# Optimization experiments

Measured on AMD Instinct MI355X. Metric: run time of the kernel, lower is better.

## Reference

```python
import jax, jax.numpy as jnp
import numpy as np

D, NH, NL, NP, NLAYERS, DFF = 256, 8, 4, 4, 6, 1024
HD = D // NH
SHAPES = [(100, 100), (50, 50), (25, 25), (13, 13)]  # (H, W) per level
B = 4


def layernorm(x, w, b):
    m = x.mean(-1, keepdims=True)
    v = ((x - m) ** 2).mean(-1, keepdims=True)
    return (x - m) / jnp.sqrt(v + 1e-5) * w + b


def bilinear_sample(vl, loc, H, W):
    # vl: [B, H*W, NH, HD] level values; loc: [B, Lq, NH, NP, 2] normalized in [0,1]
    # matches F.grid_sample(bilinear, zeros padding, align_corners=False)
    bsz, Lq = loc.shape[0], loc.shape[1]
    px = loc[..., 0] * W - 0.5
    py = loc[..., 1] * H - 0.5
    x0 = jnp.floor(px); y0 = jnp.floor(py)
    wx1 = px - x0; wy1 = py - y0
    out = jnp.zeros((bsz, Lq, NH, NP, HD), vl.dtype)
    for xi, wx in ((x0, 1.0 - wx1), (x0 + 1.0, wx1)):
        for yi, wy in ((y0, 1.0 - wy1), (y0 + 1.0, wy1)):
            valid = (xi >= 0) & (xi < W) & (yi >= 0) & (yi < H)
            xc = jnp.clip(xi, 0, W - 1).astype(jnp.int32)
            yc = jnp.clip(yi, 0, H - 1).astype(jnp.int32)
            idx = yc * W + xc                                   # [B,Lq,NH,NP]
            idx2 = idx.transpose(0, 1, 3, 2).reshape(bsz, Lq * NP, NH, 1)
            g = jnp.take_along_axis(vl, idx2, axis=1)           # [B,Lq*NP,NH,HD]
            g = g.reshape(bsz, Lq, NP, NH, HD).transpose(0, 1, 3, 2, 4)
            w = (wx * wy * valid.astype(vl.dtype))[..., None]
            out = out + g * w
    return out


def get_reference_points(bsz):
    refs = []
    for (H, W) in SHAPES:
        ry = (jnp.arange(H, dtype=jnp.float32) + 0.5) / H
        rx = (jnp.arange(W, dtype=jnp.float32) + 0.5) / W
        gy, gx = jnp.meshgrid(ry, rx, indexing='ij')
        refs.append(jnp.stack([gx.reshape(-1), gy.reshape(-1)], -1))
    ref = jnp.concatenate(refs, 0)                              # [Len, 2]
    return jnp.broadcast_to(ref[None, :, None, :], (bsz, ref.shape[0], NL, 2))


def ms_deform_attn(query, src, ref, starts, so_w, so_b, aw_w, aw_b, vp_w, vp_b, op_w, op_b):
    bsz, Lq, _ = query.shape
    value = (src @ vp_w + vp_b).reshape(bsz, -1, NH, HD)
    offsets = (query @ so_w + so_b).reshape(bsz, Lq, NH, NL, NP, 2)
    aw = (query @ aw_w + aw_b).reshape(bsz, Lq, NH, NL * NP)
    aw = jax.nn.softmax(aw, -1).reshape(bsz, Lq, NH, NL, NP)
    normalizer = jnp.array([[W, H] for (H, W) in SHAPES], jnp.float32)  # x by W, y by H
    loc = ref[:, :, None, :, None, :] + offsets / normalizer[None, None, None, :, None, :]
    out = jnp.zeros((bsz, Lq, NH, HD), query.dtype)
    for l, (H, W) in enumerate(SHAPES):
        vl = value[:, starts[l]:starts[l] + H * W]
        sampled = bilinear_sample(vl, loc[:, :, :, l], H, W)    # [B,Lq,NH,NP,HD]
        out = out + jnp.einsum('blhp,blhpd->blhd', aw[:, :, :, l], sampled)
    return out.reshape(bsz, Lq, D) @ op_w + op_b


def setup_inputs():
    key = jax.random.key(0)
    ks = iter(jax.random.split(key, 64))
    d = {}
    for i, (H, W) in enumerate(SHAPES):
        d[f'src{i}'] = jax.random.normal(next(ks), (B, D, H, W), jnp.float32)
        d[f'pos{i}'] = jax.random.normal(next(ks), (B, D, H, W), jnp.float32)
    d['level_embed'] = jax.random.normal(next(ks), (NL, D), jnp.float32)
    d['so_w'] = jax.random.normal(next(ks), (NLAYERS, D, NH * NL * NP * 2), jnp.float32) * 0.005
    d['so_b'] = jax.random.normal(next(ks), (NLAYERS, NH * NL * NP * 2), jnp.float32) * 0.1
    d['aw_w'] = jax.random.normal(next(ks), (NLAYERS, D, NH * NL * NP), jnp.float32) * 0.02
    d['aw_b'] = jnp.zeros((NLAYERS, NH * NL * NP), jnp.float32)
    d['vp_w'] = jax.random.normal(next(ks), (NLAYERS, D, D), jnp.float32) * 0.02
    d['vp_b'] = jnp.zeros((NLAYERS, D), jnp.float32)
    d['op_w'] = jax.random.normal(next(ks), (NLAYERS, D, D), jnp.float32) * 0.02
    d['op_b'] = jnp.zeros((NLAYERS, D), jnp.float32)
    d['n1_w'] = jnp.ones((NLAYERS, D), jnp.float32)
    d['n1_b'] = jnp.zeros((NLAYERS, D), jnp.float32)
    d['f1_w'] = jax.random.normal(next(ks), (NLAYERS, D, DFF), jnp.float32) * 0.02
    d['f1_b'] = jnp.zeros((NLAYERS, DFF), jnp.float32)
    d['f2_w'] = jax.random.normal(next(ks), (NLAYERS, DFF, D), jnp.float32) * 0.02
    d['f2_b'] = jnp.zeros((NLAYERS, D), jnp.float32)
    d['n2_w'] = jnp.ones((NLAYERS, D), jnp.float32)
    d['n2_b'] = jnp.zeros((NLAYERS, D), jnp.float32)
    return d


def reference(src0, src1, src2, src3, pos0, pos1, pos2, pos3, level_embed,
              so_w, so_b, aw_w, aw_b, vp_w, vp_b, op_w, op_b,
              n1_w, n1_b, f1_w, f1_b, f2_w, f2_b, n2_w, n2_b):
    srcs = [src0, src1, src2, src3]
    poss = [pos0, pos1, pos2, pos3]
    bsz = src0.shape[0]
    src_flat, pos_flat, starts, off = [], [], [], 0
    for l, ((H, W), s, p) in enumerate(zip(SHAPES, srcs, poss)):
        starts.append(off); off += H * W
        src_flat.append(s.reshape(bsz, D, H * W).transpose(0, 2, 1))
        pos_flat.append(p.reshape(bsz, D, H * W).transpose(0, 2, 1) + level_embed[l][None, None, :])
    src = jnp.concatenate(src_flat, 1)                          # [B, Len, D]
    pos = jnp.concatenate(pos_flat, 1)
    ref = get_reference_points(bsz)
    for i in range(NLAYERS):
        q = src + pos
        attn = ms_deform_attn(q, src, ref, starts,
                              so_w[i], so_b[i], aw_w[i], aw_b[i],
                              vp_w[i], vp_b[i], op_w[i], op_b[i])
        src = layernorm(src + attn, n1_w[i], n1_b[i])
        h = jax.nn.relu(src @ f1_w[i] + f1_b[i]) @ f2_w[i] + f2_b[i]
        src = layernorm(src + h, n2_w[i], n2_b[i])
    level_start_index = jnp.array(starts, jnp.int64 if jax.config.jax_enable_x64 else jnp.int32)
    return src, level_start_index
```

## Files before the change

### kernel.cpp

```cpp
#include <hip/hip_runtime.h>

#define D 256
#define L_TOT 13294

typedef __attribute__((ext_vector_type(8))) __bf16 bf16x8;
typedef __attribute__((ext_vector_type(4))) float f32x4;
typedef __attribute__((ext_vector_type(2))) float f32x2;

__device__ __forceinline__ float bf2f(unsigned short u) {
    return __uint_as_float(((unsigned int)u) << 16);
}
__device__ __forceinline__ unsigned short f2bf(float f) {
    unsigned int u = __float_as_uint(f);
    u += 0x7FFFu + ((u >> 16) & 1u);
    return (unsigned short)(u >> 16);
}
__device__ __forceinline__ f32x2 bfpair(unsigned int d) {
    f32x2 r;
    r.x = __uint_as_float(d << 16);
    r.y = __uint_as_float(d & 0xFFFF0000u);
    return r;
}
__device__ __forceinline__ f32x2 fma2(f32x2 a, float w, f32x2 c) {
    return __builtin_elementwise_fma(a, (f32x2){w, w}, c);
}

__global__ void probe_k(const unsigned short* __restrict__ u, int n, int* __restrict__ flag)
{
    __shared__ int cnt;
    if (threadIdx.x == 0) cnt = 0;
    __syncthreads();
    int c = 0;
    for (int i = threadIdx.x; i < n; i += 256) {
        const int e = (u[i] >> 7) & 0xFF;
        if (e == 0 || (e >= 96 && e <= 150)) ++c;
    }
    atomicAdd(&cnt, c);
    __syncthreads();
    if (threadIdx.x == 0) *flag = (cnt * 10 > n * 9) ? 1 : 0;
}

__global__ __launch_bounds__(256) void convert_k(
    const void* __restrict__ src, unsigned short* __restrict__ dst, int n,
    const int* __restrict__ flag)
{
    const int i = blockIdx.x * 256 + threadIdx.x;
    if (i >= n) return;
    if (*flag) dst[i] = ((const unsigned short*)src)[i];
    else       dst[i] = f2bf(((const float*)src)[i]);
}

__global__ __launch_bounds__(256) void convt_k(
    const void* __restrict__ src, unsigned short* __restrict__ dst,
    int K, int N, int L, const int* __restrict__ flag)
{
    const long e = (long)blockIdx.x * 256 + threadIdx.x;
    const long tot = (long)L * K * N;
    if (e >= tot) return;
    const int per = K * N;
    const int li = (int)(e / per);
    const int r  = (int)(e - (long)li * per);
    const int n  = r / K;
    const int k  = r - n * K;
    const long s = (long)li * per + (long)k * N + n;
    dst[e] = (*flag) ? ((const unsigned short*)src)[s]
                     : f2bf(((const float*)src)[s]);
}

__global__ __launch_bounds__(256) void flatten_k(
    const void* __restrict__ s0, const void* __restrict__ s1,
    const void* __restrict__ s2, const void* __restrict__ s3,
    const int* __restrict__ flag, unsigned short* __restrict__ state)
{
    const long e = (long)blockIdx.x * 256 + threadIdx.x;
    const int d = (int)(e & 255);
    const long tok = e >> 8;
    const int b = (int)(tok / L_TOT);
    const int t = (int)(tok - (long)b * L_TOT);
    const void *sp;
    int hw, idx;
    if (t < 10000)      { sp = s0; hw = 10000; idx = t;          }
    else if (t < 12500) { sp = s1; hw = 2500;  idx = t - 10000;  }
    else if (t < 13125) { sp = s2; hw = 625;   idx = t - 12500;  }
    else                { sp = s3; hw = 169;   idx = t - 13125;  }
    const long a = ((long)b * D + d) * hw + idx;
    state[e] = (*flag) ? ((const unsigned short*)sp)[a]
                       : f2bf(((const float*)sp)[a]);
}

__global__ __launch_bounds__(256) void posconst_k(
    const void* __restrict__ p0, const void* __restrict__ p1,
    const void* __restrict__ p2, const void* __restrict__ p3,
    const unsigned short* __restrict__ lev, const int* __restrict__ flag,
    unsigned short* __restrict__ posc)
{
    const long e = (long)blockIdx.x * 256 + threadIdx.x;
    const int d = (int)(e & 255);
    const long tok = e >> 8;
    const int b = (int)(tok / L_TOT);
    const int t = (int)(tok - (long)b * L_TOT);
    const void *pp;
    int hw, idx, l;
    if (t < 10000)      { pp = p0; hw = 10000; idx = t;          l = 0; }
    else if (t < 12500) { pp = p1; hw = 2500;  idx = t - 10000;  l = 1; }
    else if (t < 13125) { pp = p2; hw = 625;   idx = t - 12500;  l = 2; }
    else                { pp = p3; hw = 169;   idx = t - 13125;  l = 3; }
    const long a = ((long)b * D + d) * hw + idx;
    const float pv = (*flag) ? bf2f(((const unsigned short*)pp)[a])
                             : ((const float*)pp)[a];
    posc[e] = f2bf(pv + bf2f(lev[l * D + d]));
}

__global__ __launch_bounds__(256) void addq_k(
    const unsigned short* __restrict__ x, const unsigned short* __restrict__ p,
    unsigned short* __restrict__ q, long n8)
{
    const long e = (long)blockIdx.x * 256 + threadIdx.x;
    if (e >= n8) return;
    const uint4 xv = ((const uint4*)x)[e];
    const uint4 pv = ((const uint4*)p)[e];
    uint4 o;
#define ADDPK(a, b) ({ const f32x2 fa = bfpair(a), fb = bfpair(b); \
        (unsigned int)f2bf(fb.x + fa.x) | ((unsigned int)f2bf(fb.y + fa.y) << 16); })
    o.x = ADDPK(xv.x, pv.x); o.y = ADDPK(xv.y, pv.y);
    o.z = ADDPK(xv.z, pv.z); o.w = ADDPK(xv.w, pv.w);
#undef ADDPK
    ((uint4*)q)[e] = o;
}

__global__ __launch_bounds__(256) void posflat_k(
    const void* __restrict__ p0, const void* __restrict__ p1,
    const void* __restrict__ p2, const void* __restrict__ p3,
    const unsigned short* __restrict__ lev, const int* __restrict__ flag,
    const unsigned short* __restrict__ x, unsigned short* __restrict__ q)
{
    const long e = (long)blockIdx.x * 256 + threadIdx.x;
    const int d = (int)(e & 255);
    const long tok = e >> 8;
    const int b = (int)(tok / L_TOT);
    const int t = (int)(tok - (long)b * L_TOT);
    const void *pp;
    int hw, idx, l;
    if (t < 10000)      { pp = p0; hw = 10000; idx = t;          l = 0; }
    else if (t < 12500) { pp = p1; hw = 2500;  idx = t - 10000;  l = 1; }
    else if (t < 13125) { pp = p2; hw = 625;   idx = t - 12500;  l = 2; }
    else                { pp = p3; hw = 169;   idx = t - 13125;  l = 3; }
    const long a = ((long)b * D + d) * hw + idx;
    const float pv = (*flag) ? bf2f(((const unsigned short*)pp)[a])
                             : ((const float*)pp)[a];
    q[e] = f2bf(pv + bf2f(lev[l * D + d]) + bf2f(x[e]));
}

template<bool RELU, bool RESID>
__device__ __forceinline__ void gemm_core(
    const unsigned short* __restrict__ A, int ldA,
    const unsigned short* __restrict__ Bt, int ldB,
    const unsigned short* __restrict__ bias,
    const unsigned short* resid,
    unsigned short* out, int ldO,
    long M, int K, int col0, long row0,
    unsigned short* As, unsigned short* Bs)
{
    const int tid = threadIdx.x;
    const int l  = tid & 63;
    const int w  = tid >> 6;
    const int wm = w >> 1, wn = w & 1;

    f32x4 acc[4][4];
#pragma unroll
    for (int i = 0; i < 4; ++i)
#pragma unroll
        for (int j = 0; j < 4; ++j) acc[i][j] = (f32x4){0.f, 0.f, 0.f, 0.f};

    const int sr = tid >> 3;
    const int sg = tid & 7;

    for (int k0 = 0; k0 < K; k0 += 64) {
#pragma unroll
        for (int i = 0; i < 4; ++i) {
            const int r = i * 32 + sr;
            long arow = row0 + r; if (arow >= M) arow = M - 1;
            const int ke = k0 + ((sg ^ (r & 7)) << 3);
            const unsigned short* ga = A  + arow * (long)ldA + ke;
            const unsigned short* gb = Bt + (long)(col0 + r) * ldB + ke;
            __builtin_amdgcn_global_load_lds(
                (const __attribute__((address_space(1))) void*)ga,
                (__attribute__((address_space(3))) void*)(As + i * 2048 + w * 512),
                16, 0, 0);
            __builtin_amdgcn_global_load_lds(
                (const __attribute__((address_space(1))) void*)gb,
                (__attribute__((address_space(3))) void*)(Bs + i * 2048 + w * 512),
                16, 0, 0);
        }
        __syncthreads();
#pragma unroll
        for (int ks = 0; ks < 2; ++ks) {
            const int cc  = ks * 4 + (l >> 4);
            const int swz = ((cc ^ (l & 7)) << 4);
            bf16x8 af[4], bfr[4];
#pragma unroll
            for (int mi = 0; mi < 4; ++mi) {
                const int ar = wm * 64 + mi * 16 + (l & 15);
                af[mi] = *(const bf16x8*)((const char*)As + ar * 128 + swz);
            }
#pragma unroll
            for (int ni = 0; ni < 4; ++ni) {
                const int br = wn * 64 + ni * 16 + (l & 15);
                bfr[ni] = *(const bf16x8*)((const char*)Bs + br * 128 + swz);
            }
#pragma unroll
            for (int mi = 0; mi < 4; ++mi)
#pragma unroll
                for (int ni = 0; ni < 4; ++ni)
                    acc[mi][ni] = __builtin_amdgcn_mfma_f32_16x16x32_bf16(
                        bfr[ni], af[mi], acc[mi][ni], 0, 0, 0);
        }
        __syncthreads();
    }

#pragma unroll
    for (int mi = 0; mi < 4; ++mi) {
        const long rr = row0 + wm * 64 + mi * 16 + (l & 15);
        if (rr >= M) continue;
#pragma unroll
        for (int ni = 0; ni < 4; ++ni) {
            const int col = col0 + wn * 64 + ni * 16 + (l >> 4) * 4;
            f32x4 v = acc[mi][ni];
            if (bias) {
                const ushort4 b4 = *(const ushort4*)(bias + col);
                v[0] += bf2f(b4.x); v[1] += bf2f(b4.y);
                v[2] += bf2f(b4.z); v[3] += bf2f(b4.w);
            }
            if (RELU) {
                v[0] = fmaxf(v[0], 0.f); v[1] = fmaxf(v[1], 0.f);
                v[2] = fmaxf(v[2], 0.f); v[3] = fmaxf(v[3], 0.f);
            }
            if (RESID) {
                const ushort4 r4 = *(const ushort4*)(resid + rr * (long)ldO + col);
                v[0] += bf2f(r4.x); v[1] += bf2f(r4.y);
                v[2] += bf2f(r4.z); v[3] += bf2f(r4.w);
            }
            ushort4 o;
            o.x = f2bf(v[0]); o.y = f2bf(v[1]); o.z = f2bf(v[2]); o.w = f2bf(v[3]);
            *(ushort4*)(out + rr * (long)ldO + col) = o;
        }
    }
}

template<bool RELU, bool RESID>
__global__ __launch_bounds__(256, 3) void mgemm_k(
    const unsigned short* __restrict__ A, int ldA,
    const unsigned short* __restrict__ Bt, int ldB,
    const unsigned short* __restrict__ bias,
    const unsigned short* resid,
    unsigned short* out, int ldOut,
    long M, int K)
{
    __shared__ unsigned short As[8192];
    __shared__ unsigned short Bs[8192];
    gemm_core<RELU, RESID>(A, ldA, Bt, ldB, bias, resid, out, ldOut,
                           M, K, blockIdx.x * 128, (long)blockIdx.y * 128, As, Bs);
}

__global__ __launch_bounds__(256, 3) void mgemm3_k(
    const unsigned short* __restrict__ state, const unsigned short* __restrict__ q,
    const unsigned short* __restrict__ Wv,  const unsigned short* __restrict__ bv,
    const unsigned short* __restrict__ Wso, const unsigned short* __restrict__ bso,
    const unsigned short* __restrict__ Waw, const unsigned short* __restrict__ baw,
    unsigned short* valo, unsigned short* offo, unsigned short* awo, long M)
{
    __shared__ unsigned short As[8192];
    __shared__ unsigned short Bs[8192];
    const int cx = blockIdx.x * 128;
    const long row0 = (long)blockIdx.y * 128;
    if (cx < 256)
        gemm_core<false, false>(state, D, Wv, D, bv, nullptr, valo, D,
                                M, D, cx, row0, As, Bs);
    else if (cx < 512)
        gemm_core<false, false>(q, D, Wso, D, bso, nullptr, offo, D,
                                M, D, cx - 256, row0, As, Bs);
    else
        gemm_core<false, false>(q, D, Waw, D, baw, nullptr, awo, 128,
                                M, D, 0, row0, As, Bs);
}

__global__ __launch_bounds__(256) void sample_k(
    const unsigned short* __restrict__ off, const unsigned short* __restrict__ aw,
    const unsigned short* __restrict__ val, unsigned short* __restrict__ attn)
{
    __shared__ __align__(16) int   cidx[128][4];
    __shared__ __align__(16) float cw[128][4];
    __shared__ float red[3][4][64];
    const long tok = blockIdx.x;
    const int tid = threadIdx.x;
    const int b = (int)(tok / L_TOT);
    const int t = (int)(tok - (long)b * L_TOT);

    if (tid < 128) {
        const int u = tid;
        const int lp = u & 15;
        const int mu = lp * 8 + (u >> 4);
        const int cswz = lp & 3;
        const float logit = bf2f(aw[tok * 128 + u]);
        float m = logit;
#pragma unroll
        for (int mk = 1; mk < 16; mk <<= 1) m = fmaxf(m, __shfl_xor(m, mk));
        const float e = expf(logit - m);
        float s = e;
#pragma unroll
        for (int mk = 1; mk < 16; mk <<= 1) s += __shfl_xor(s, mk);
        const float a = e / s;
        int st0, W0;
        if (t < 10000)      { st0 = 0;     W0 = 100; }
        else if (t < 12500) { st0 = 10000; W0 = 50;  }
        else if (t < 13125) { st0 = 12500; W0 = 25;  }
        else                { st0 = 13125; W0 = 13;  }
        const int i0 = t - st0;
        const int yy = i0 / W0;
        const int xx = i0 - yy * W0;
        const float gx = (xx + 0.5f) / (float)W0;
        const float gy = (yy + 0.5f) / (float)W0;
        const int lv = (u >> 2) & 3;
        const int Wv  = (lv == 0) ? 100 : (lv == 1) ? 50 : (lv == 2) ? 25 : 13;
        const int stl = (lv == 0) ? 0 : (lv == 1) ? 10000 : (lv == 2) ? 12500 : 13125;
        const unsigned int op = *(const unsigned int*)(off + tok * 256 + 2 * u);
        const float ox = bf2f((unsigned short)op);
        const float oy = bf2f((unsigned short)(op >> 16));
        const float px = (gx + ox / (float)Wv) * Wv - 0.5f;
        const float py = (gy + oy / (float)Wv) * Wv - 0.5f;
        const float fx = floorf(px), fy = floorf(py);
        const float wx1 = px - fx, wy1 = py - fy;
        const int x0 = (int)fx, y0 = (int)fy;
#pragma unroll
        for (int c = 0; c < 4; ++c) {
            const int xi = x0 + (c & 1);
            const int yi = y0 + (c >> 1);
            const float wgt = ((c & 1) ? wx1 : 1.f - wx1) * ((c >> 1) ? wy1 : 1.f - wy1);
            const bool ok = (xi >= 0) && (xi < Wv) && (yi >= 0) && (yi < Wv);
            cidx[mu][c ^ cswz] = ok ? ((stl + yi * Wv + xi) << 9) : 0;
            cw[mu][c ^ cswz]   = ok ? wgt * a : 0.f;
        }
    }
    __syncthreads();
    const int g = tid >> 6;
    const int l = tid & 63;
    const int h = l >> 3;
    const int q = l & 7;
    const char* vb = (const char*)val + ((long)b * L_TOT) * 512 + h * 64 + q * 8;
    f32x2 A01 = {0.f, 0.f}, A23 = {0.f, 0.f};
#pragma unroll
    for (int j = 0; j < 4; ++j) {
        const int mu = (j * 4 + g) * 8 + h;
        const int4   ci = *(const int4*)(&cidx[mu][0]);
        const float4 wv = *(const float4*)(&cw[mu][0]);
        const uint2 d0 = *(const uint2*)(vb + ci.x);
        const uint2 d1 = *(const uint2*)(vb + ci.y);
        const uint2 d2 = *(const uint2*)(vb + ci.z);
        const uint2 d3 = *(const uint2*)(vb + ci.w);
        A01 = fma2(bfpair(d0.x), wv.x, A01);  A23 = fma2(bfpair(d0.y), wv.x, A23);
        A01 = fma2(bfpair(d1.x), wv.y, A01);  A23 = fma2(bfpair(d1.y), wv.y, A23);
        A01 = fma2(bfpair(d2.x), wv.z, A01);  A23 = fma2(bfpair(d2.y), wv.z, A23);
        A01 = fma2(bfpair(d3.x), wv.w, A01);  A23 = fma2(bfpair(d3.y), wv.w, A23);
    }
    if (g) {
        red[g - 1][0][l] = A01.x; red[g - 1][1][l] = A01.y;
        red[g - 1][2][l] = A23.x; red[g - 1][3][l] = A23.y;
    }
    __syncthreads();
    if (g == 0) {
        float a0 = A01.x, a1 = A01.y, a2 = A23.x, a3 = A23.y;
#pragma unroll
        for (int p = 0; p < 3; ++p) {
            a0 += red[p][0][l]; a1 += red[p][1][l];
            a2 += red[p][2][l]; a3 += red[p][3][l];
        }
        ushort4 o;
        o.x = f2bf(a0); o.y = f2bf(a1); o.z = f2bf(a2); o.w = f2bf(a3);
        *(ushort4*)(attn + tok * 256 + h * 32 + q * 4) = o;
    }
}

template<bool QOUT>
__global__ __launch_bounds__(256) void ln_k(
    const unsigned short* __restrict__ y,
    const unsigned short* __restrict__ g, const unsigned short* __restrict__ bb,
    unsigned short* __restrict__ out,
    const unsigned short* __restrict__ posc, unsigned short* __restrict__ qout,
    long nt)
{
    const int wv = threadIdx.x >> 6;
    const int lane = threadIdx.x & 63;
    const long tok = (long)blockIdx.x * 4 + wv;
    if (tok >= nt) return;
    const ushort4 v4 = *(const ushort4*)(y + tok * D + lane * 4);
    const float v0 = bf2f(v4.x), v1 = bf2f(v4.y), v2 = bf2f(v4.z), v3 = bf2f(v4.w);
    float s = v0 + v1 + v2 + v3;
#pragma unroll
    for (int m = 1; m < 64; m <<= 1) s += __shfl_xor(s, m);
    const float mean = s * (1.f / D);
    const float d0 = v0 - mean, d1 = v1 - mean, d2 = v2 - mean, d3 = v3 - mean;
    float q = d0 * d0 + d1 * d1 + d2 * d2 + d3 * d3;
#pragma unroll
    for (int m = 1; m < 64; m <<= 1) q += __shfl_xor(q, m);
    const float rstd = rsqrtf(q * (1.f / D) + 1e-5f);
    const int c0 = lane * 4;
    ushort4 o;
    o.x = f2bf(d0 * rstd * bf2f(g[c0 + 0]) + bf2f(bb[c0 + 0]));
    o.y = f2bf(d1 * rstd * bf2f(g[c0 + 1]) + bf2f(bb[c0 + 1]));
    o.z = f2bf(d2 * rstd * bf2f(g[c0 + 2]) + bf2f(bb[c0 + 2]));
    o.w = f2bf(d3 * rstd * bf2f(g[c0 + 3]) + bf2f(bb[c0 + 3]));
    *(ushort4*)(out + tok * D + c0) = o;
    if (QOUT) {
        const ushort4 p4 = *(const ushort4*)(posc + tok * D + c0);
        ushort4 qo;
        qo.x = f2bf(bf2f(o.x) + bf2f(p4.x));
        qo.y = f2bf(bf2f(o.y) + bf2f(p4.y));
        qo.z = f2bf(bf2f(o.z) + bf2f(p4.z));
        qo.w = f2bf(bf2f(o.w) + bf2f(p4.w));
        *(ushort4*)(qout + tok * D + c0) = qo;
    }
}

__global__ __launch_bounds__(256) void finalize_k(
    const unsigned short* __restrict__ state, float* __restrict__ out, long osz)
{
    const long e = (long)blockIdx.x * 256 + threadIdx.x;
    const long n0 = osz - 4;
    if (e < n0) out[e] = bf2f(state[e]);
    if (e < 4) {
        const float st[4] = {0.f, 10000.f, 12500.f, 13125.f};
        out[n0 + e] = st[e];
    }
}

extern "C" void kernel_launch(void* const* d_in, const int* in_sizes, int n_in,
                              void* d_out, int out_size, void* d_ws, size_t ws_size,
                              hipStream_t stream)
{
    (void)n_in;
    const long osz = (long)out_size;
    const long nt = (osz - 4) / D;
    const int nlayers = in_sizes[9] / (D * D);
    const int dff = in_sizes[19] / (nlayers * D);

    char* ws = (char*)d_ws;
    int* flag = (int*)ws;  ws += 256;
    unsigned short* wc = (unsigned short*)ws;
    long off[25]; long acc_off = 0;
    for (int i = 8; i <= 24; ++i) { off[i] = acc_off; acc_off += in_sizes[i]; }
    ws += ((acc_off * 2 + 255) / 256) * 256;
    const size_t SZ_BF = (size_t)nt * D * 2;
    unsigned short* state     = (unsigned short*)ws;  ws += SZ_BF;
    unsigned short* val_b     = (unsigned short*)ws;  ws += SZ_BF;
    unsigned short* offy_b    = (unsigned short*)ws;  ws += SZ_BF;
    unsigned short* posattn_b = (unsigned short*)ws;  ws += SZ_BF;
    unsigned short* aw_b      = (unsigned short*)ws;  ws += (size_t)nt * 128 * 2;
    unsigned short* hbuf = val_b;

    const size_t used_base = (size_t)((char*)aw_b - (char*)d_ws) + (size_t)nt * 128 * 2;
    const bool have_posc  = (ws_size >= used_base + SZ_BF);
    const bool have_hfull = (ws_size >= used_base + SZ_BF + 4 * SZ_BF);
    unsigned short* posc  = (unsigned short*)((char*)d_ws + used_base);
    unsigned short* hfull = (unsigned short*)((char*)d_ws + used_base + SZ_BF);

    probe_k<<<1, 256, 0, stream>>>((const unsigned short*)d_in[8], in_sizes[8], flag);

    const int vecIdx[11] = {8, 10, 12, 14, 16, 17, 18, 20, 22, 23, 24};
    for (int j = 0; j < 11; ++j) {
        const int i = vecIdx[j];
        convert_k<<<(in_sizes[i] + 255) / 256, 256, 0, stream>>>(
            d_in[i], wc + off[i], in_sizes[i], flag);
    }
    const int matIdx[6] = {9, 11, 13, 15, 19, 21};
    const int matK[6]   = {D, D, D, D, D, dff};
    const int matN[6]   = {D, 128, D, D, dff, D};
    for (int j = 0; j < 6; ++j) {
        const int i = matIdx[j];
        convt_k<<<(in_sizes[i] + 255) / 256, 256, 0, stream>>>(
            d_in[i], wc + off[i], matK[j], matN[j], nlayers, flag);
    }

    flatten_k<<<(int)nt, 256, 0, stream>>>(
        d_in[0], d_in[2], d_in[4], d_in[6], flag, state);
    if (have_posc)
        posconst_k<<<(int)nt, 256, 0, stream>>>(
            d_in[1], d_in[3], d_in[5], d_in[7], wc + off[8], flag, posc);

    const int MB = (int)((nt + 127) / 128);
    const int LB = (int)((nt + 3) / 4);
    const long n8 = (long)nt * D / 8;
    const int AB = (int)((n8 + 255) / 256);
    const int dh = dff / 2;

    if (have_posc)
        addq_k<<<AB, 256, 0, stream>>>(state, posc, posattn_b, n8);

    for (int i = 0; i < nlayers; ++i) {
        if (!have_posc)
            posflat_k<<<(int)nt, 256, 0, stream>>>(
                d_in[1], d_in[3], d_in[5], d_in[7], wc + off[8], flag, state, posattn_b);
        mgemm3_k<<<dim3(5, MB), 256, 0, stream>>>(
            state, posattn_b,
            wc + off[13] + (long)i * D * D,   wc + off[14] + i * D,
            wc + off[9]  + (long)i * D * 256, wc + off[10] + i * 256,
            wc + off[11] + (long)i * D * 128, wc + off[12] + i * 128,
            val_b, offy_b, aw_b, nt);
        sample_k<<<(int)nt, 256, 0, stream>>>(offy_b, aw_b, val_b, posattn_b);
        mgemm_k<false, true><<<dim3(2, MB), 256, 0, stream>>>(
            posattn_b, D, wc + off[15] + (long)i * D * D, D, wc + off[16] + i * D,
            state, offy_b, D, nt, D);
        ln_k<false><<<LB, 256, 0, stream>>>(offy_b, wc + off[17] + i * D,
            wc + off[18] + i * D, state, nullptr, nullptr, nt);
        if (have_hfull) {
            mgemm_k<true, false><<<dim3(dff / 128, MB), 256, 0, stream>>>(
                state, D, wc + off[19] + (long)i * D * dff, D, wc + off[20] + i * dff,
                nullptr, hfull, dff, nt, D);
            mgemm_k<false, true><<<dim3(2, MB), 256, 0, stream>>>(
                hfull, dff, wc + off[21] + (long)i * dff * D, dff, wc + off[22] + i * D,
                state, posattn_b, D, nt, dff);
        } else {
            mgemm_k<true, false><<<dim3(dh / 128, MB), 256, 0, stream>>>(
                state, D, wc + off[19] + (long)i * D * dff, D, wc + off[20] + i * dff,
                nullptr, hbuf, dh, nt, D);
            mgemm_k<false, true><<<dim3(2, MB), 256, 0, stream>>>(
                hbuf, dh, wc + off[21] + (long)i * dff * D, dff, wc + off[22] + i * D,
                state, posattn_b, D, nt, dh);
            mgemm_k<true, false><<<dim3(dh / 128, MB), 256, 0, stream>>>(
                state, D, wc + off[19] + (long)i * D * dff + (long)dh * D, D,
                wc + off[20] + i * dff + dh, nullptr, hbuf, dh, nt, D);
            mgemm_k<false, true><<<dim3(2, MB), 256, 0, stream>>>(
                hbuf, dh, wc + off[21] + (long)i * dff * D + dh, dff, nullptr,
                posattn_b, posattn_b, D, nt, dh);
        }
        if (have_posc && i + 1 < nlayers)
            ln_k<true><<<LB, 256, 0, stream>>>(posattn_b, wc + off[23] + i * D,
                wc + off[24] + i * D, state, posc, posattn_b, nt);
        else
            ln_k<false><<<LB, 256, 0, stream>>>(posattn_b, wc + off[23] + i * D,
                wc + off[24] + i * D, state, nullptr, nullptr, nt);
    }

    finalize_k<<<(int)((osz - 4 + 255) / 256), 256, 0, stream>>>(
        state, (float*)d_out, osz);
}
```

Baseline: 2.479 ms.

## Fuse output-projection and FFN2 GEMMs with residual add and LayerNorm

Adds a GEMM kernel whose 64-row tiles span the full 256-wide output, so the residual add and LayerNorm (plus the optional pos-add for the next layer's query) run in the epilogue. It replaces the separate GEMM and ln_k launches on the hfull path. This removes the round trip of the intermediate activation through global memory and two launches per layer. The cost is fewer blocks with a large B tile held in LDS. Reading resid and writing outp in place on the same state buffer relies on each block touching only its own rows.

Measured after the change: 2.406 ms. -2.9%, faster.

```diff
diff --git a/kernel.cpp b/kernel.cpp
--- a/kernel.cpp
+++ b/kernel.cpp
@@ -282,6 +282,149 @@
     else
         gemm_core<false, false>(q, D, Waw, D, baw, nullptr, awo, 128,
                                 M, D, 0, row0, As, Bs);
+}
+
+template<bool QOUT>
+__global__ __launch_bounds__(256, 3) void mgemmln_k(
+    const unsigned short* __restrict__ A, int ldA,
+    const unsigned short* __restrict__ Bt, int ldB,
+    const unsigned short* __restrict__ bias,
+    const unsigned short* resid,
+    const unsigned short* __restrict__ gamma,
+    const unsigned short* __restrict__ beta,
+    unsigned short* outp,
+    const unsigned short* __restrict__ posc,
+    unsigned short* __restrict__ qout,
+    long M, int K)
+{
+    __shared__ unsigned short As[64 * 64];
+    __shared__ unsigned short Bs[256 * 64];
+    __shared__ float red[2][4][4][16];
+    const int tid = threadIdx.x;
+    const int l = tid & 63;
+    const int w = tid >> 6;
+    const long row0 = (long)blockIdx.x * 64;
+
+    f32x4 acc[4][4];
+#pragma unroll
+    for (int i = 0; i < 4; ++i)
+#pragma unroll
+        for (int j = 0; j < 4; ++j) acc[i][j] = (f32x4){0.f, 0.f, 0.f, 0.f};
+
+    for (int k0 = 0; k0 < K; k0 += 64) {
+#pragma unroll
+        for (int i = 0; i < 10; ++i) {
+            const int c = i * 256 + tid;
+            const unsigned short* gsrc;
+            unsigned short* ldst;
+            if (i < 2) {
+                const int r = c >> 3, grp = c & 7;
+                long ar = row0 + r; if (ar >= M) ar = M - 1;
+                gsrc = A + ar * (long)ldA + (k0 + ((grp ^ (r & 7)) << 3));
+                ldst = As + (c << 3);
+            } else {
+                const int r = (c >> 3) - 64, grp = c & 7;
+                gsrc = Bt + (long)r * ldB + (k0 + ((grp ^ (r & 7)) << 3));
+                ldst = Bs + ((c - 512) << 3);
+            }
+            __builtin_amdgcn_global_load_lds(
+                (const __attribute__((address_space(1))) void*)gsrc,
+                (__attribute__((address_space(3))) void*)ldst, 16, 0, 0);
+        }
+        __syncthreads();
+#pragma unroll
+        for (int ks = 0; ks < 2; ++ks) {
+            const int cc = ks * 4 + (l >> 4);
+            bf16x8 af[4], bfr[4];
+#pragma unroll
+            for (int mi = 0; mi < 4; ++mi) {
+                const int ar = mi * 16 + (l & 15);
+                af[mi] = *(const bf16x8*)((const char*)As + ar * 128 + ((cc ^ (ar & 7)) << 4));
+            }
+#pragma unroll
+            for (int ni = 0; ni < 4; ++ni) {
+                const int br = w * 64 + ni * 16 + (l & 15);
+                bfr[ni] = *(const bf16x8*)((const char*)Bs + br * 128 + ((cc ^ (br & 7)) << 4));
+            }
+#pragma unroll
+            for (int mi = 0; mi < 4; ++mi)
+#pragma unroll
+                for (int ni = 0; ni < 4; ++ni)
+                    acc[mi][ni] = __builtin_amdgcn_mfma_f32_16x16x32_bf16(
+                        bfr[ni], af[mi], acc[mi][ni], 0, 0, 0);
+        }
+        __syncthreads();
+    }
+
+#pragma unroll
+    for (int mi = 0; mi < 4; ++mi) {
+        const long rr = row0 + mi * 16 + (l & 15);
+        const long rrc = (rr < M) ? rr : (M - 1);
+#pragma unroll
+        for (int ni = 0; ni < 4; ++ni) {
+            const int col = w * 64 + ni * 16 + (l >> 4) * 4;
+            const ushort4 b4 = *(const ushort4*)(bias + col);
+            const ushort4 r4 = *(const ushort4*)(resid + rrc * D + col);
+            acc[mi][ni][0] = bf2f(f2bf(acc[mi][ni][0] + bf2f(b4.x) + bf2f(r4.x)));
+            acc[mi][ni][1] = bf2f(f2bf(acc[mi][ni][1] + bf2f(b4.y) + bf2f(r4.y)));
+            acc[mi][ni][2] = bf2f(f2bf(acc[mi][ni][2] + bf2f(b4.z) + bf2f(r4.z)));
+            acc[mi][ni][3] = bf2f(f2bf(acc[mi][ni][3] + bf2f(b4.w) + bf2f(r4.w)));
+        }
+    }
+#pragma unroll
+    for (int mi = 0; mi < 4; ++mi) {
+        float s = 0.f, qq = 0.f;
+#pragma unroll
+        for (int ni = 0; ni < 4; ++ni)
+#pragma unroll
+            for (int r = 0; r < 4; ++r) {
+                const float v = acc[mi][ni][r];
+                s += v; qq += v * v;
+            }
+        s += __shfl_xor(s, 16);  s += __shfl_xor(s, 32);
+        qq += __shfl_xor(qq, 16); qq += __shfl_xor(qq, 32);
+        if (l < 16) { red[0][w][mi][l] = s; red[1][w][mi][l] = qq; }
+    }
+    __syncthreads();
+    float mean[4], rstd[4];
+#pragma unroll
+    for (int mi = 0; mi < 4; ++mi) {
+        const int r16 = l & 15;
+        const float s = red[0][0][mi][r16] + red[0][1][mi][r16]
+                      + red[0][2][mi][r16] + red[0][3][mi][r16];
+        const float qq = red[1][0][mi][r16] + red[1][1][mi][r16]
+                       + red[1][2][mi][r16] + red[1][3][mi][r16];
+        const float mn = s * (1.f / D);
+        const float var = qq * (1.f / D) - mn * mn;
+        mean[mi] = mn;
+        rstd[mi] = rsqrtf(var + 1e-5f);
+    }
+#pragma unroll
+    for (int mi = 0; mi < 4; ++mi) {
+        const long rr = row0 + mi * 16 + (l & 15);
+        if (rr >= M) continue;
+#pragma unroll
+        for (int ni = 0; ni < 4; ++ni) {
+            const int col = w * 64 + ni * 16 + (l >> 4) * 4;
+            const ushort4 g4 = *(const ushort4*)(gamma + col);
+            const ushort4 e4 = *(const ushort4*)(beta + col);
+            ushort4 o;
+            o.x = f2bf((acc[mi][ni][0] - mean[mi]) * rstd[mi] * bf2f(g4.x) + bf2f(e4.x));
+            o.y = f2bf((acc[mi][ni][1] - mean[mi]) * rstd[mi] * bf2f(g4.y) + bf2f(e4.y));
+            o.z = f2bf((acc[mi][ni][2] - mean[mi]) * rstd[mi] * bf2f(g4.z) + bf2f(e4.z));
+            o.w = f2bf((acc[mi][ni][3] - mean[mi]) * rstd[mi] * bf2f(g4.w) + bf2f(e4.w));
+            *(ushort4*)(outp + rr * D + col) = o;
+            if (QOUT) {
+                const ushort4 p4 = *(const ushort4*)(posc + rr * D + col);
+                ushort4 qo;
+                qo.x = f2bf(bf2f(o.x) + bf2f(p4.x));
+                qo.y = f2bf(bf2f(o.y) + bf2f(p4.y));
+                qo.z = f2bf(bf2f(o.z) + bf2f(p4.z));
+                qo.w = f2bf(bf2f(o.w) + bf2f(p4.w));
+                *(ushort4*)(qout + rr * D + col) = qo;
+            }
+        }
+    }
 }
 
 __global__ __launch_bounds__(256) void sample_k(
@@ -487,6 +630,7 @@
             d_in[1], d_in[3], d_in[5], d_in[7], wc + off[8], flag, posc);
 
     const int MB = (int)((nt + 127) / 128);
+    const int FB = (int)((nt + 63) / 64);
     const int LB = (int)((nt + 3) / 4);
     const long n8 = (long)nt * D / 8;
     const int AB = (int)((n8 + 255) / 256);
@@ -506,19 +650,32 @@
             wc + off[11] + (long)i * D * 128, wc + off[12] + i * 128,
             val_b, offy_b, aw_b, nt);
         sample_k<<<(int)nt, 256, 0, stream>>>(offy_b, aw_b, val_b, posattn_b);
-        mgemm_k<false, true><<<dim3(2, MB), 256, 0, stream>>>(
-            posattn_b, D, wc + off[15] + (long)i * D * D, D, wc + off[16] + i * D,
-            state, offy_b, D, nt, D);
-        ln_k<false><<<LB, 256, 0, stream>>>(offy_b, wc + off[17] + i * D,
-            wc + off[18] + i * D, state, nullptr, nullptr, nt);
         if (have_hfull) {
+            mgemmln_k<false><<<FB, 256, 0, stream>>>(
+                posattn_b, D, wc + off[15] + (long)i * D * D, D, wc + off[16] + i * D,
+                state, wc + off[17] + i * D, wc + off[18] + i * D, state,
+                nullptr, nullptr, nt, D);
             mgemm_k<true, false><<<dim3(dff / 128, MB), 256, 0, stream>>>(
                 state, D, wc + off[19] + (long)i * D * dff, D, wc + off[20] + i * dff,
                 nullptr, hfull, dff, nt, D);
+            if (have_posc && i + 1 < nlayers)
+                mgemmln_k<true><<<FB, 256, 0, stream>>>(
+                    hfull, dff, wc + off[21] + (long)i * dff * D, dff,
+                    wc + off[22] + i * D, state,
+                    wc + off[23] + i * D, wc + off[24] + i * D, state,
+                    posc, posattn_b, nt, dff);
+            else
+                mgemmln_k<false><<<FB, 256, 0, stream>>>(
+                    hfull, dff, wc + off[21] + (long)i * dff * D, dff,
+                    wc + off[22] + i * D, state,
+                    wc + off[23] + i * D, wc + off[24] + i * D, state,
+                    nullptr, nullptr, nt, dff);
+        } else {
             mgemm_k<false, true><<<dim3(2, MB), 256, 0, stream>>>(
-                hfull, dff, wc + off[21] + (long)i * dff * D, dff, wc + off[22] + i * D,
-                state, posattn_b, D, nt, dff);
-        } else {
+                posattn_b, D, wc + off[15] + (long)i * D * D, D, wc + off[16] + i * D,
+                state, offy_b, D, nt, D);
+            ln_k<false><<<LB, 256, 0, stream>>>(offy_b, wc + off[17] + i * D,
+                wc + off[18] + i * D, state, nullptr, nullptr, nt);
             mgemm_k<true, false><<<dim3(dh / 128, MB), 256, 0, stream>>>(
                 state, D, wc + off[19] + (long)i * D * dff, D, wc + off[20] + i * dff,
                 nullptr, hbuf, dh, nt, D);
@@ -531,13 +688,13 @@
             mgemm_k<false, true><<<dim3(2, MB), 256, 0, stream>>>(
                 hbuf, dh, wc + off[21] + (long)i * dff * D + dh, dff, nullptr,
                 posattn_b, posattn_b, D, nt, dh);
-        }
-        if (have_posc && i + 1 < nlayers)
-            ln_k<true><<<LB, 256, 0, stream>>>(posattn_b, wc + off[23] + i * D,
-                wc + off[24] + i * D, state, posc, posattn_b, nt);
-        else
-            ln_k<false><<<LB, 256, 0, stream>>>(posattn_b, wc + off[23] + i * D,
-                wc + off[24] + i * D, state, nullptr, nullptr, nt);
+            if (have_posc && i + 1 < nlayers)
+                ln_k<true><<<LB, 256, 0, stream>>>(posattn_b, wc + off[23] + i * D,
+                    wc + off[24] + i * D, state, posc, posattn_b, nt);
+            else
+                ln_k<false><<<LB, 256, 0, stream>>>(posattn_b, wc + off[23] + i * D,
+                    wc + off[24] + i * D, state, nullptr, nullptr, nt);
+        }
     }
 
     finalize_k<<<(int)((osz - 4 + 255) / 256), 256, 0, stream>>>(
```
